# Kernel tuning notes

Measured on AMD Instinct MI355X. Metric: run time of the kernel, lower is better.

Reference implementation:

```python
import jax, jax.numpy as jnp
import numpy as np

B, S, D = 4, 2048, 1024
H, HD = 16, 64
MLP = 4 * D
EPS = 1e-6


def _rms_norm(x, scale):
    var = jnp.mean(jnp.square(x), axis=-1, keepdims=True)
    return x * jax.lax.rsqrt(var + EPS) * scale


def setup_inputs() -> dict:
    key = jax.random.key(0)
    ks = jax.random.split(key, 8)
    sd = D ** -0.5
    return {
        "x": jax.random.normal(ks[0], (B, S, D), jnp.float32),
        "pre_norm_scale": jnp.ones((D,), jnp.float32),
        "w_mlp_in": jax.random.normal(ks[1], (D, MLP), jnp.float32) * sd,   # MLPBlockInput, no bias
        "wq": jax.random.normal(ks[2], (D, H, HD), jnp.float32) * sd,
        "wk": jax.random.normal(ks[3], (D, H, HD), jnp.float32) * sd,
        "wv": jax.random.normal(ks[4], (D, H, HD), jnp.float32) * sd,
        "w_mlp_out": jax.random.normal(ks[5], (MLP, D), jnp.float32) * (MLP ** -0.5),
        "b_mlp_out": jnp.zeros((D,), jnp.float32),
        "w_attn_out": jax.random.normal(ks[6], (H, HD, D), jnp.float32) * sd,  # DenseGeneral axis=(-2,-1)
        "b_attn_out": jnp.zeros((D,), jnp.float32),
    }


def reference(x, pre_norm_scale, w_mlp_in, wq, wk, wv, w_mlp_out, b_mlp_out,
              w_attn_out, b_attn_out):
    residual = x
    xn = _rms_norm(x, pre_norm_scale)                      # pre_norm (TPNorm)

    # QKVMLPDense: fused MLP-input + QKV projections
    h = jax.nn.gelu(jnp.einsum("bsd,df->bsf", xn, w_mlp_in))   # [B,S,MLP]
    q = jnp.einsum("bsd,dhk->bshk", xn, wq)                    # [B,S,H,HD]
    k = jnp.einsum("bsd,dhk->bshk", xn, wk)
    v = jnp.einsum("bsd,dhk->bshk", xn, wv)

    # dot_product_attention (mask=None)
    scores = jnp.einsum("bqhd,bkhd->bhqk", q, k) / jnp.sqrt(jnp.asarray(HD, x.dtype))
    probs = jax.nn.softmax(scores, axis=-1)
    attn_v = jnp.einsum("bhqk,bkhd->bqhd", probs, v)           # [B,S,H,HD]

    # AttnMLPOut: mlp_out + attn_out
    mlp_out = jnp.einsum("bsf,fd->bsd", h, w_mlp_out) + b_mlp_out
    attn_out = jnp.einsum("bqhk,hkd->bqd", attn_v, w_attn_out) + b_attn_out
    block_out = mlp_out + attn_out                              # dropout is identity (train=False)
    return residual + block_out
```

## Files before the change

kernel.cpp:

```cpp
#include <hip/hip_runtime.h>
#include <cstdint>
#include <cstddef>

typedef float floatx4 __attribute__((ext_vector_type(4)));
typedef short bf16x8 __attribute__((ext_vector_type(8)));

#define MFMA(a, b, c) __builtin_amdgcn_mfma_f32_16x16x32_bf16((a), (b), (c), 0, 0, 0)

__device__ __forceinline__ unsigned short f2bf(float f) {
  union { float f; unsigned int u; } v; v.f = f;
  unsigned int u = v.u;
  unsigned int r = (u + 0x7FFFu + ((u >> 16) & 1u)) >> 16;
  return (unsigned short)r;
}

__device__ __forceinline__ void gload_lds16(const unsigned short* g, unsigned short* s) {
  __builtin_amdgcn_global_load_lds(
      (const __attribute__((address_space(1))) unsigned int*)g,
      (__attribute__((address_space(3))) unsigned int*)s, 16, 0, 0);
}

__device__ __forceinline__ float gelu_f(float v) {
  float z = 0.7978845608028654f * (v + 0.044715f * v * v * v);
  float e = __expf(2.0f * z);
  float th = 1.0f - 2.0f / (e + 1.0f);
  return 0.5f * v * (1.0f + th);
}

__global__ __launch_bounds__(256) void prep_all(
    const float* __restrict__ w_mlp_in, const float* __restrict__ wq,
    const float* __restrict__ wk, const float* __restrict__ wv,
    const float* __restrict__ w_mlp_out, const float* __restrict__ w_attn_out,
    const float* __restrict__ x, const float* __restrict__ pns,
    unsigned short* __restrict__ wcatT, unsigned short* __restrict__ wcat2T,
    unsigned short* __restrict__ xn) {
  __shared__ float tile[32][33];
  __shared__ float ws4[4];
  int id = blockIdx.x;
  if (id >= 12288) {
    int row = id - 12288;
    const float4 v = ((const float4*)(x + (size_t)row * 1024))[threadIdx.x];
    float ss = v.x * v.x + v.y * v.y + v.z * v.z + v.w * v.w;
#pragma unroll
    for (int off = 1; off < 64; off <<= 1) ss += __shfl_xor(ss, off, 64);
    if ((threadIdx.x & 63) == 0) ws4[threadIdx.x >> 6] = ss;
    __syncthreads();
    float tot = ws4[0] + ws4[1] + ws4[2] + ws4[3];
    float rs = rsqrtf(tot * (1.0f / 1024.0f) + 1e-6f);
    const float4 sc = ((const float4*)pns)[threadIdx.x];
    uint2 o;
    o.x = (unsigned)f2bf(v.x * rs * sc.x) | ((unsigned)f2bf(v.y * rs * sc.y) << 16);
    o.y = (unsigned)f2bf(v.z * rs * sc.z) | ((unsigned)f2bf(v.w * rs * sc.w) << 16);
    ((uint2*)(xn + (size_t)row * 1024))[threadIdx.x] = o;
    return;
  }
  const float* src; unsigned short* dst; int C, ldd, bx, by, q;
  if (id < 4096)       { src = w_mlp_in;   dst = wcatT;                        C = 4096; ldd = 1024; q = id;         bx = q & 127; by = q >> 7; }
  else if (id < 5120)  { src = wq;         dst = wcatT + (size_t)4096 * 1024;  C = 1024; ldd = 1024; q = id - 4096;  bx = q & 31;  by = q >> 5; }
  else if (id < 6144)  { src = wk;         dst = wcatT + (size_t)5120 * 1024;  C = 1024; ldd = 1024; q = id - 5120;  bx = q & 31;  by = q >> 5; }
  else if (id < 7168)  { src = wv;         dst = wcatT + (size_t)6144 * 1024;  C = 1024; ldd = 1024; q = id - 6144;  bx = q & 31;  by = q >> 5; }
  else if (id < 11264) { src = w_mlp_out;  dst = wcat2T;                       C = 1024; ldd = 5120; q = id - 7168;  bx = q & 31;  by = q >> 5; }
  else                 { src = w_attn_out; dst = wcat2T + 4096;                C = 1024; ldd = 5120; q = id - 11264; bx = q & 31;  by = q >> 5; }
  int tx = threadIdx.x & 31, ty = threadIdx.x >> 5;
#pragma unroll
  for (int i = 0; i < 4; i++) {
    int r = ty + i * 8;
    tile[r][tx] = src[(size_t)(by * 32 + r) * C + bx * 32 + tx];
  }
  __syncthreads();
#pragma unroll
  for (int i = 0; i < 4; i++) {
    int r = ty + i * 8;
    dst[(size_t)(bx * 32 + r) * ldd + by * 32 + tx] = f2bf(tile[tx][r]);
  }
}

template <int MODE>
__global__ __launch_bounds__(256, 2) void gemm_bt(
    const unsigned short* __restrict__ A, const unsigned short* __restrict__ BT,
    int K, void* __restrict__ outp,
    const float* __restrict__ bias1, const float* __restrict__ bias2,
    const float* __restrict__ resid,
    int msplit, int tm, int tn,
    unsigned short* __restrict__ q_out, unsigned short* __restrict__ k_out,
    unsigned short* __restrict__ v_out) {
  __shared__ unsigned short As[2][128 * 32];
  __shared__ unsigned short Bs[2][128 * 32];

  int id = blockIdx.x + gridDim.x * blockIdx.y;
  int xcd = id & 7, j = id >> 3;
  int mh = xcd % msplit, nq = xcd / msplit;
  int by = mh * tm + j / tn;
  int bx = nq * tn + j % tn;
  int m0 = by * 128, n0 = bx * 128;

  int t = threadIdx.x, lane = t & 63, wave = t >> 6;
  int l15 = lane & 15, quad = lane >> 4;
  int wm = (wave & 1) * 64, wn = (wave >> 1) * 64;

  floatx4 acc[4][4] = {};

  int lr = lane >> 2;
  int lg = (lane & 3) ^ ((lane >> 3) & 3);
  int ch0 = wave * 2, ch1 = wave * 2 + 1;
  const unsigned short* gA0 = A + (size_t)(m0 + ch0 * 16 + lr) * K + lg * 8;
  const unsigned short* gA1 = A + (size_t)(m0 + ch1 * 16 + lr) * K + lg * 8;
  const unsigned short* gB0 = BT + (size_t)(n0 + ch0 * 16 + lr) * K + lg * 8;
  const unsigned short* gB1 = BT + (size_t)(n0 + ch1 * 16 + lr) * K + lg * 8;
  unsigned short* sA0[2] = {&As[0][ch0 * 512 + lane * 8], &As[1][ch0 * 512 + lane * 8]};
  unsigned short* sA1[2] = {&As[0][ch1 * 512 + lane * 8], &As[1][ch1 * 512 + lane * 8]};
  unsigned short* sB0[2] = {&Bs[0][ch0 * 512 + lane * 8], &Bs[1][ch0 * 512 + lane * 8]};
  unsigned short* sB1[2] = {&Bs[0][ch1 * 512 + lane * 8], &Bs[1][ch1 * 512 + lane * 8]};

  int fo = (4 * l15 + (quad ^ ((l15 >> 1) & 3))) * 8;
  int ca = (wm >> 4);
  int cb = (wn >> 4);

  for (int kt = 0; kt < K; kt += 64) {
    __syncthreads();
#pragma unroll
    for (int kk = 0; kk < 2; kk++) {
      int kg = kt + kk * 32;
      gload_lds16(gA0 + kg, sA0[kk]);
      gload_lds16(gA1 + kg, sA1[kk]);
      gload_lds16(gB0 + kg, sB0[kk]);
      gload_lds16(gB1 + kg, sB1[kk]);
    }
    __syncthreads();
#pragma unroll
    for (int kk = 0; kk < 2; kk++) {
      bf16x8 a[4], b[4];
#pragma unroll
      for (int im = 0; im < 4; im++)
        a[im] = *(const bf16x8*)&As[kk][(ca + im) * 512 + fo];
#pragma unroll
      for (int in_ = 0; in_ < 4; in_++)
        b[in_] = *(const bf16x8*)&Bs[kk][(cb + in_) * 512 + fo];
#pragma unroll
      for (int im = 0; im < 4; im++)
#pragma unroll
        for (int in_ = 0; in_ < 4; in_++)
          acc[im][in_] = MFMA(a[im], b[in_], acc[im][in_]);
    }
  }

#pragma unroll
  for (int im = 0; im < 4; im++) {
#pragma unroll
    for (int in_ = 0; in_ < 4; in_++) {
      int row0 = m0 + wm + im * 16 + quad * 4;
      int col = n0 + wn + in_ * 16 + l15;
      if constexpr (MODE == 6) {
        if (n0 < 4096) {
#pragma unroll
          for (int r = 0; r < 4; r++) {
            __builtin_nontemporal_store(f2bf(gelu_f(acc[im][in_][r])),
                &((unsigned short*)outp)[(size_t)(row0 + r) * 5120 + col]);
          }
        } else {
          int seg = (n0 - 4096) >> 10;
          int cs = col - 4096 - (seg << 10);
          int h = cs >> 6, hd = cs & 63;
          int b_ = row0 >> 11, s0 = row0 & 2047;
          if (seg == 2) {
            unsigned long long o =
                (unsigned long long)((unsigned)f2bf(acc[im][in_][0]) |
                                     ((unsigned)f2bf(acc[im][in_][1]) << 16)) |
                ((unsigned long long)((unsigned)f2bf(acc[im][in_][2]) |
                                      ((unsigned)f2bf(acc[im][in_][3]) << 16)) << 32);
            __builtin_nontemporal_store(o,
                (unsigned long long*)&v_out[(((size_t)(b_ * 16 + h)) * 64 + hd) * 2048 + s0]);
          } else {
            float sc = (seg == 0) ? 0.125f : 1.0f;
            unsigned short* dst = (seg == 0) ? q_out : k_out;
#pragma unroll
            for (int r = 0; r < 4; r++) {
              __builtin_nontemporal_store(f2bf(acc[im][in_][r] * sc),
                  &dst[(((size_t)(b_ * 16 + h)) * 2048 + s0 + r) * 64 + hd]);
            }
          }
        }
      } else {
        float bsum = bias1[col] + bias2[col];
#pragma unroll
        for (int r = 0; r < 4; r++) {
          size_t idx = (size_t)(row0 + r) * 1024 + col;
          float res = __builtin_nontemporal_load(&resid[idx]);
          __builtin_nontemporal_store(acc[im][in_][r] + bsum + res, &((float*)outp)[idx]);
        }
      }
    }
  }
}

__global__ __launch_bounds__(256, 2) void flash_attn(
    const unsigned short* __restrict__ q_buf, const unsigned short* __restrict__ k_buf,
    const unsigned short* __restrict__ v_buf, unsigned short* __restrict__ cat) {
  constexpr int S = 2048, HD = 64;
  constexpr int LK = 72, LV = 72, LP = 68;
  __shared__ unsigned short Ks[64 * LK];
  __shared__ unsigned short Vs[64 * LV];
  __shared__ unsigned short Ps[4][32 * LP];

  int id = blockIdx.x + gridDim.x * blockIdx.y;
  int xcd = id & 7, j = id >> 3;
  int bh = xcd * 8 + (j >> 4);
  int qbk = j & 15;

  int t = threadIdx.x, lane = t & 63, wave = t >> 6;
  int l15 = lane & 15, quad = lane >> 4;

  const unsigned short* qp = q_buf + (size_t)bh * S * HD;
  const unsigned short* kp = k_buf + (size_t)bh * S * HD;
  const unsigned short* vp = v_buf + (size_t)bh * HD * S;

  int q0 = qbk * 128 + wave * 32;
  bf16x8 aQ[2][2];
#pragma unroll
  for (int qf = 0; qf < 2; qf++) {
    aQ[qf][0] = *(const bf16x8*)&qp[(size_t)(q0 + qf * 16 + l15) * HD + quad * 8];
    aQ[qf][1] = *(const bf16x8*)&qp[(size_t)(q0 + qf * 16 + l15) * HD + 32 + quad * 8];
  }

  floatx4 acc_o[2][4] = {};
  float lrow[2][4] = {};

  int kr = t >> 3, kc = (t & 7) * 8;

  uint4 rK0 = *(const uint4*)&kp[(size_t)kr * HD + kc];
  uint4 rK1 = *(const uint4*)&kp[(size_t)(kr + 32) * HD + kc];
  uint4 rV0 = *(const uint4*)&vp[(size_t)kr * S + kc];
  uint4 rV1 = *(const uint4*)&vp[(size_t)(kr + 32) * S + kc];

  for (int kv = 0; kv < S; kv += 64) {
    __syncthreads();
    *(uint4*)&Ks[kr * LK + kc] = rK0;
    *(uint4*)&Ks[(kr + 32) * LK + kc] = rK1;
    *(uint4*)&Vs[kr * LV + kc] = rV0;
    *(uint4*)&Vs[(kr + 32) * LV + kc] = rV1;
    __syncthreads();
    if (kv + 64 < S) {
      rK0 = *(const uint4*)&kp[(size_t)(kv + 64 + kr) * HD + kc];
      rK1 = *(const uint4*)&kp[(size_t)(kv + 64 + kr + 32) * HD + kc];
      rV0 = *(const uint4*)&vp[(size_t)kr * S + kv + 64 + kc];
      rV1 = *(const uint4*)&vp[(size_t)(kr + 32) * S + kv + 64 + kc];
    }

    floatx4 z[2][4];
#pragma unroll
    for (int cg = 0; cg < 4; cg++) {
      bf16x8 bk0 = *(const bf16x8*)&Ks[(cg * 16 + l15) * LK + quad * 8];
      bf16x8 bk1 = *(const bf16x8*)&Ks[(cg * 16 + l15) * LK + 32 + quad * 8];
#pragma unroll
      for (int qf = 0; qf < 2; qf++) {
        floatx4 acc = {};
        acc = MFMA(aQ[qf][0], bk0, acc);
        acc = MFMA(aQ[qf][1], bk1, acc);
        z[qf][cg] = acc;
      }
    }
#pragma unroll
    for (int qf = 0; qf < 2; qf++)
#pragma unroll
      for (int cg = 0; cg < 4; cg++)
#pragma unroll
        for (int r = 0; r < 4; r++) {
          float e = __expf(z[qf][cg][r]);
          lrow[qf][r] += e;
          Ps[wave][(qf * 16 + quad * 4 + r) * LP + cg * 16 + l15] = f2bf(e);
        }
    asm volatile("s_waitcnt lgkmcnt(0)" ::: "memory");
#pragma unroll
    for (int c = 0; c < 2; c++) {
      bf16x8 aP[2];
#pragma unroll
      for (int qf = 0; qf < 2; qf++) {
        const unsigned short* pp = &Ps[wave][(qf * 16 + l15) * LP + c * 32 + quad * 8];
        ((uint2*)&aP[qf])[0] = *(const uint2*)pp;
        ((uint2*)&aP[qf])[1] = *(const uint2*)(pp + 4);
      }
#pragma unroll
      for (int n = 0; n < 4; n++) {
        bf16x8 bv = *(const bf16x8*)&Vs[(n * 16 + l15) * LV + c * 32 + quad * 8];
        acc_o[0][n] = MFMA(aP[0], bv, acc_o[0][n]);
        acc_o[1][n] = MFMA(aP[1], bv, acc_o[1][n]);
      }
    }
  }

#pragma unroll
  for (int qf = 0; qf < 2; qf++)
#pragma unroll
    for (int r = 0; r < 4; r++) {
      float s = lrow[qf][r];
#pragma unroll
      for (int off = 1; off < 16; off <<= 1) s += __shfl_xor(s, off, 16);
      lrow[qf][r] = s;
    }

  int b_ = bh >> 4, h = bh & 15;
#pragma unroll
  for (int qf = 0; qf < 2; qf++)
#pragma unroll
    for (int r = 0; r < 4; r++) {
      float inv = 1.0f / lrow[qf][r];
      int srow = q0 + qf * 16 + quad * 4 + r;
      size_t base = ((size_t)(b_ * 2048 + srow)) * 5120 + 4096 + h * 64;
#pragma unroll
      for (int n = 0; n < 4; n++)
        cat[base + n * 16 + l15] = f2bf(acc_o[qf][n][r] * inv);
    }
}

extern "C" void kernel_launch(void* const* d_in, const int* in_sizes, int n_in,
                              void* d_out, int out_size, void* d_ws, size_t ws_size,
                              hipStream_t stream) {
  (void)in_sizes; (void)n_in; (void)out_size; (void)ws_size;
  const float* x          = (const float*)d_in[0];
  const float* pns        = (const float*)d_in[1];
  const float* w_mlp_in   = (const float*)d_in[2];
  const float* wq         = (const float*)d_in[3];
  const float* wk         = (const float*)d_in[4];
  const float* wv         = (const float*)d_in[5];
  const float* w_mlp_out  = (const float*)d_in[6];
  const float* b_mlp_out  = (const float*)d_in[7];
  const float* w_attn_out = (const float*)d_in[8];
  const float* b_attn_out = (const float*)d_in[9];
  float* out = (float*)d_out;

  char* ws = (char*)d_ws;
  size_t off = 0;
  auto alloc = [&](size_t bytes) {
    void* p = ws + off;
    off += (bytes + 255) & ~(size_t)255;
    return p;
  };
  const size_t M = 8192;
  unsigned short* xn     = (unsigned short*)alloc(M * 1024 * 2);
  unsigned short* wcatT  = (unsigned short*)alloc((size_t)7168 * 1024 * 2);
  unsigned short* wcat2T = (unsigned short*)alloc((size_t)1024 * 5120 * 2);
  unsigned short* cat    = (unsigned short*)alloc(M * 5120 * 2);
  unsigned short* qb     = (unsigned short*)alloc(M * 1024 * 2);
  unsigned short* kb     = (unsigned short*)alloc(M * 1024 * 2);
  unsigned short* vb     = (unsigned short*)alloc(M * 1024 * 2);

  prep_all<<<dim3(20480), 256, 0, stream>>>(
      w_mlp_in, wq, wk, wv, w_mlp_out, w_attn_out, x, pns, wcatT, wcat2T, xn);

  gemm_bt<6><<<dim3(56, 64), 256, 0, stream>>>(
      xn, wcatT, 1024, cat, nullptr, nullptr, nullptr, 2, 32, 14, qb, kb, vb);

  flash_attn<<<dim3(16, 64), 256, 0, stream>>>(qb, kb, vb, cat);

  gemm_bt<7><<<dim3(8, 64), 256, 0, stream>>>(
      cat, wcat2T, 5120, out, b_mlp_out, b_attn_out, x, 2, 32, 2, nullptr, nullptr, nullptr);
}
```

Baseline: 520.7 us.

## Split QKV GEMM out and co-schedule MLP-in GEMM with flash attention

```diff
diff --git a/kernel.cpp b/kernel.cpp
--- a/kernel.cpp
+++ b/kernel.cpp
@@ -76,6 +76,119 @@
 }
 
 template <int MODE>
+__device__ __forceinline__ void gemm_core(
+    int xcd, int j,
+    const unsigned short* __restrict__ A, const unsigned short* __restrict__ BT,
+    int K, void* __restrict__ outp,
+    const float* __restrict__ bias1, const float* __restrict__ bias2,
+    const float* __restrict__ resid,
+    int msplit, int tm, int tn,
+    unsigned short* __restrict__ q_out, unsigned short* __restrict__ k_out,
+    unsigned short* __restrict__ v_out,
+    unsigned short* As, unsigned short* Bs) {
+  int mh = xcd % msplit, nq = xcd / msplit;
+  int by = mh * tm + j / tn;
+  int bx = nq * tn + j % tn;
+  int m0 = by * 128, n0 = bx * 128;
+
+  int t = threadIdx.x, lane = t & 63, wave = t >> 6;
+  int l15 = lane & 15, quad = lane >> 4;
+  int wm = (wave & 1) * 64, wn = (wave >> 1) * 64;
+
+  floatx4 acc[4][4] = {};
+
+  int lr = lane >> 2;
+  int lg = (lane & 3) ^ ((lane >> 3) & 3);
+  int ch0 = wave * 2, ch1 = wave * 2 + 1;
+  const unsigned short* gA0 = A + (size_t)(m0 + ch0 * 16 + lr) * K + lg * 8;
+  const unsigned short* gA1 = A + (size_t)(m0 + ch1 * 16 + lr) * K + lg * 8;
+  const unsigned short* gB0 = BT + (size_t)(n0 + ch0 * 16 + lr) * K + lg * 8;
+  const unsigned short* gB1 = BT + (size_t)(n0 + ch1 * 16 + lr) * K + lg * 8;
+  unsigned short* sA0[2] = {As + ch0 * 512 + lane * 8, As + 4096 + ch0 * 512 + lane * 8};
+  unsigned short* sA1[2] = {As + ch1 * 512 + lane * 8, As + 4096 + ch1 * 512 + lane * 8};
+  unsigned short* sB0[2] = {Bs + ch0 * 512 + lane * 8, Bs + 4096 + ch0 * 512 + lane * 8};
+  unsigned short* sB1[2] = {Bs + ch1 * 512 + lane * 8, Bs + 4096 + ch1 * 512 + lane * 8};
+
+  int fo = (4 * l15 + (quad ^ ((l15 >> 1) & 3))) * 8;
+  int ca = (wm >> 4);
+  int cb = (wn >> 4);
+
+  for (int kt = 0; kt < K; kt += 64) {
+    __syncthreads();
+#pragma unroll
+    for (int kk = 0; kk < 2; kk++) {
+      int kg = kt + kk * 32;
+      gload_lds16(gA0 + kg, sA0[kk]);
+      gload_lds16(gA1 + kg, sA1[kk]);
+      gload_lds16(gB0 + kg, sB0[kk]);
+      gload_lds16(gB1 + kg, sB1[kk]);
+    }
+    __syncthreads();
+#pragma unroll
+    for (int kk = 0; kk < 2; kk++) {
+      bf16x8 a[4], b[4];
+#pragma unroll
+      for (int im = 0; im < 4; im++)
+        a[im] = *(const bf16x8*)&As[kk * 4096 + (ca + im) * 512 + fo];
+#pragma unroll
+      for (int in_ = 0; in_ < 4; in_++)
+        b[in_] = *(const bf16x8*)&Bs[kk * 4096 + (cb + in_) * 512 + fo];
+#pragma unroll
+      for (int im = 0; im < 4; im++)
+#pragma unroll
+        for (int in_ = 0; in_ < 4; in_++)
+          acc[im][in_] = MFMA(a[im], b[in_], acc[im][in_]);
+    }
+  }
+
+#pragma unroll
+  for (int im = 0; im < 4; im++) {
+#pragma unroll
+    for (int in_ = 0; in_ < 4; in_++) {
+      int row0 = m0 + wm + im * 16 + quad * 4;
+      int col = n0 + wn + in_ * 16 + l15;
+      if constexpr (MODE == 8) {
+#pragma unroll
+        for (int r = 0; r < 4; r++) {
+          __builtin_nontemporal_store(f2bf(gelu_f(acc[im][in_][r])),
+              &((unsigned short*)outp)[(size_t)(row0 + r) * 5120 + col]);
+        }
+      } else if constexpr (MODE == 9) {
+        int seg = n0 >> 10;
+        int cs = col - (seg << 10);
+        int h = cs >> 6, hd = cs & 63;
+        int b_ = row0 >> 11, s0 = row0 & 2047;
+        if (seg == 2) {
+          unsigned long long o =
+              (unsigned long long)((unsigned)f2bf(acc[im][in_][0]) |
+                                   ((unsigned)f2bf(acc[im][in_][1]) << 16)) |
+              ((unsigned long long)((unsigned)f2bf(acc[im][in_][2]) |
+                                    ((unsigned)f2bf(acc[im][in_][3]) << 16)) << 32);
+          __builtin_nontemporal_store(o,
+              (unsigned long long*)&v_out[(((size_t)(b_ * 16 + h)) * 64 + hd) * 2048 + s0]);
+        } else {
+          float sc = (seg == 0) ? 0.125f : 1.0f;
+          unsigned short* dst = (seg == 0) ? q_out : k_out;
+#pragma unroll
+          for (int r = 0; r < 4; r++) {
+            __builtin_nontemporal_store(f2bf(acc[im][in_][r] * sc),
+                &dst[(((size_t)(b_ * 16 + h)) * 2048 + s0 + r) * 64 + hd]);
+          }
+        }
+      } else {
+        float bsum = bias1[col] + bias2[col];
+#pragma unroll
+        for (int r = 0; r < 4; r++) {
+          size_t idx = (size_t)(row0 + r) * 1024 + col;
+          float res = __builtin_nontemporal_load(&resid[idx]);
+          __builtin_nontemporal_store(acc[im][in_][r] + bsum + res, &((float*)outp)[idx]);
+        }
+      }
+    }
+  }
+}
+
+template <int MODE>
 __global__ __launch_bounds__(256, 2) void gemm_bt(
     const unsigned short* __restrict__ A, const unsigned short* __restrict__ BT,
     int K, void* __restrict__ outp,
@@ -84,131 +197,30 @@
     int msplit, int tm, int tn,
     unsigned short* __restrict__ q_out, unsigned short* __restrict__ k_out,
     unsigned short* __restrict__ v_out) {
-  __shared__ unsigned short As[2][128 * 32];
-  __shared__ unsigned short Bs[2][128 * 32];
-
+  __shared__ unsigned short As[2 * 128 * 32];
+  __shared__ unsigned short Bs[2 * 128 * 32];
   int id = blockIdx.x + gridDim.x * blockIdx.y;
-  int xcd = id & 7, j = id >> 3;
-  int mh = xcd % msplit, nq = xcd / msplit;
-  int by = mh * tm + j / tn;
-  int bx = nq * tn + j % tn;
-  int m0 = by * 128, n0 = bx * 128;
+  gemm_core<MODE>(id & 7, id >> 3, A, BT, K, outp, bias1, bias2, resid,
+                  msplit, tm, tn, q_out, k_out, v_out, As, Bs);
+}
+
+__device__ __forceinline__ void flash_body(
+    int xcd, int j,
+    const unsigned short* __restrict__ q_buf, const unsigned short* __restrict__ k_buf,
+    const unsigned short* __restrict__ v_buf, unsigned short* __restrict__ cat,
+    unsigned short* smem) {
+  constexpr int S = 2048, HD = 64;
+  constexpr int LK = 72, LV = 72, LP = 68;
+  unsigned short* Ks = smem;
+  unsigned short* Vs = smem + 4608;
+  unsigned short* Psb = smem + 9216;
+
+  int bh = xcd * 8 + (j >> 4);
+  int qbk = j & 15;
 
   int t = threadIdx.x, lane = t & 63, wave = t >> 6;
   int l15 = lane & 15, quad = lane >> 4;
-  int wm = (wave & 1) * 64, wn = (wave >> 1) * 64;
-
-  floatx4 acc[4][4] = {};
-
-  int lr = lane >> 2;
-  int lg = (lane & 3) ^ ((lane >> 3) & 3);
-  int ch0 = wave * 2, ch1 = wave * 2 + 1;
-  const unsigned short* gA0 = A + (size_t)(m0 + ch0 * 16 + lr) * K + lg * 8;
-  const unsigned short* gA1 = A + (size_t)(m0 + ch1 * 16 + lr) * K + lg * 8;
-  const unsigned short* gB0 = BT + (size_t)(n0 + ch0 * 16 + lr) * K + lg * 8;
-  const unsigned short* gB1 = BT + (size_t)(n0 + ch1 * 16 + lr) * K + lg * 8;
-  unsigned short* sA0[2] = {&As[0][ch0 * 512 + lane * 8], &As[1][ch0 * 512 + lane * 8]};
-  unsigned short* sA1[2] = {&As[0][ch1 * 512 + lane * 8], &As[1][ch1 * 512 + lane * 8]};
-  unsigned short* sB0[2] = {&Bs[0][ch0 * 512 + lane * 8], &Bs[1][ch0 * 512 + lane * 8]};
-  unsigned short* sB1[2] = {&Bs[0][ch1 * 512 + lane * 8], &Bs[1][ch1 * 512 + lane * 8]};
-
-  int fo = (4 * l15 + (quad ^ ((l15 >> 1) & 3))) * 8;
-  int ca = (wm >> 4);
-  int cb = (wn >> 4);
-
-  for (int kt = 0; kt < K; kt += 64) {
-    __syncthreads();
-#pragma unroll
-    for (int kk = 0; kk < 2; kk++) {
-      int kg = kt + kk * 32;
-      gload_lds16(gA0 + kg, sA0[kk]);
-      gload_lds16(gA1 + kg, sA1[kk]);
-      gload_lds16(gB0 + kg, sB0[kk]);
-      gload_lds16(gB1 + kg, sB1[kk]);
-    }
-    __syncthreads();
-#pragma unroll
-    for (int kk = 0; kk < 2; kk++) {
-      bf16x8 a[4], b[4];
-#pragma unroll
-      for (int im = 0; im < 4; im++)
-        a[im] = *(const bf16x8*)&As[kk][(ca + im) * 512 + fo];
-#pragma unroll
-      for (int in_ = 0; in_ < 4; in_++)
-        b[in_] = *(const bf16x8*)&Bs[kk][(cb + in_) * 512 + fo];
-#pragma unroll
-      for (int im = 0; im < 4; im++)
-#pragma unroll
-        for (int in_ = 0; in_ < 4; in_++)
-          acc[im][in_] = MFMA(a[im], b[in_], acc[im][in_]);
-    }
-  }
-
-#pragma unroll
-  for (int im = 0; im < 4; im++) {
-#pragma unroll
-    for (int in_ = 0; in_ < 4; in_++) {
-      int row0 = m0 + wm + im * 16 + quad * 4;
-      int col = n0 + wn + in_ * 16 + l15;
-      if constexpr (MODE == 6) {
-        if (n0 < 4096) {
-#pragma unroll
-          for (int r = 0; r < 4; r++) {
-            __builtin_nontemporal_store(f2bf(gelu_f(acc[im][in_][r])),
-                &((unsigned short*)outp)[(size_t)(row0 + r) * 5120 + col]);
-          }
-        } else {
-          int seg = (n0 - 4096) >> 10;
-          int cs = col - 4096 - (seg << 10);
-          int h = cs >> 6, hd = cs & 63;
-          int b_ = row0 >> 11, s0 = row0 & 2047;
-          if (seg == 2) {
-            unsigned long long o =
-                (unsigned long long)((unsigned)f2bf(acc[im][in_][0]) |
-                                     ((unsigned)f2bf(acc[im][in_][1]) << 16)) |
-                ((unsigned long long)((unsigned)f2bf(acc[im][in_][2]) |
-                                      ((unsigned)f2bf(acc[im][in_][3]) << 16)) << 32);
-            __builtin_nontemporal_store(o,
-                (unsigned long long*)&v_out[(((size_t)(b_ * 16 + h)) * 64 + hd) * 2048 + s0]);
-          } else {
-            float sc = (seg == 0) ? 0.125f : 1.0f;
-            unsigned short* dst = (seg == 0) ? q_out : k_out;
-#pragma unroll
-            for (int r = 0; r < 4; r++) {
-              __builtin_nontemporal_store(f2bf(acc[im][in_][r] * sc),
-                  &dst[(((size_t)(b_ * 16 + h)) * 2048 + s0 + r) * 64 + hd]);
-            }
-          }
-        }
-      } else {
-        float bsum = bias1[col] + bias2[col];
-#pragma unroll
-        for (int r = 0; r < 4; r++) {
-          size_t idx = (size_t)(row0 + r) * 1024 + col;
-          float res = __builtin_nontemporal_load(&resid[idx]);
-          __builtin_nontemporal_store(acc[im][in_][r] + bsum + res, &((float*)outp)[idx]);
-        }
-      }
-    }
-  }
-}
-
-__global__ __launch_bounds__(256, 2) void flash_attn(
-    const unsigned short* __restrict__ q_buf, const unsigned short* __restrict__ k_buf,
-    const unsigned short* __restrict__ v_buf, unsigned short* __restrict__ cat) {
-  constexpr int S = 2048, HD = 64;
-  constexpr int LK = 72, LV = 72, LP = 68;
-  __shared__ unsigned short Ks[64 * LK];
-  __shared__ unsigned short Vs[64 * LV];
-  __shared__ unsigned short Ps[4][32 * LP];
-
-  int id = blockIdx.x + gridDim.x * blockIdx.y;
-  int xcd = id & 7, j = id >> 3;
-  int bh = xcd * 8 + (j >> 4);
-  int qbk = j & 15;
-
-  int t = threadIdx.x, lane = t & 63, wave = t >> 6;
-  int l15 = lane & 15, quad = lane >> 4;
+  unsigned short* Ps = Psb + wave * (32 * LP);
 
   const unsigned short* qp = q_buf + (size_t)bh * S * HD;
   const unsigned short* kp = k_buf + (size_t)bh * S * HD;
@@ -267,7 +279,7 @@
         for (int r = 0; r < 4; r++) {
           float e = __expf(z[qf][cg][r]);
           lrow[qf][r] += e;
-          Ps[wave][(qf * 16 + quad * 4 + r) * LP + cg * 16 + l15] = f2bf(e);
+          Ps[(qf * 16 + quad * 4 + r) * LP + cg * 16 + l15] = f2bf(e);
         }
     asm volatile("s_waitcnt lgkmcnt(0)" ::: "memory");
 #pragma unroll
@@ -275,7 +287,7 @@
       bf16x8 aP[2];
 #pragma unroll
       for (int qf = 0; qf < 2; qf++) {
-        const unsigned short* pp = &Ps[wave][(qf * 16 + l15) * LP + c * 32 + quad * 8];
+        const unsigned short* pp = &Ps[(qf * 16 + l15) * LP + c * 32 + quad * 8];
         ((uint2*)&aP[qf])[0] = *(const uint2*)pp;
         ((uint2*)&aP[qf])[1] = *(const uint2*)(pp + 4);
       }
@@ -310,6 +322,23 @@
       for (int n = 0; n < 4; n++)
         cat[base + n * 16 + l15] = f2bf(acc_o[qf][n][r] * inv);
     }
+}
+
+__global__ __launch_bounds__(256, 2) void fused_mlp_attn(
+    const unsigned short* __restrict__ xn, const unsigned short* __restrict__ wcatT,
+    unsigned short* __restrict__ cat,
+    const unsigned short* __restrict__ qb, const unsigned short* __restrict__ kb,
+    const unsigned short* __restrict__ vb) {
+  __shared__ __align__(16) unsigned short smem[17920];
+  int phys = blockIdx.x;
+  int xcd = phys & 7, r = phys >> 3;
+  if (r % 3 == 2) {
+    flash_body(xcd, r / 3, qb, kb, vb, cat, smem);
+  } else {
+    int g = (r / 3) * 2 + (r % 3);
+    gemm_core<8>(xcd, g, xn, wcatT, 1024, cat, nullptr, nullptr, nullptr,
+                 2, 32, 8, nullptr, nullptr, nullptr, smem, smem + 8192);
+  }
 }
 
 extern "C" void kernel_launch(void* const* d_in, const int* in_sizes, int n_in,
@@ -347,10 +376,11 @@
   prep_all<<<dim3(20480), 256, 0, stream>>>(
       w_mlp_in, wq, wk, wv, w_mlp_out, w_attn_out, x, pns, wcatT, wcat2T, xn);
 
-  gemm_bt<6><<<dim3(56, 64), 256, 0, stream>>>(
-      xn, wcatT, 1024, cat, nullptr, nullptr, nullptr, 2, 32, 14, qb, kb, vb);
-
-  flash_attn<<<dim3(16, 64), 256, 0, stream>>>(qb, kb, vb, cat);
+  gemm_bt<9><<<dim3(1536), 256, 0, stream>>>(
+      xn, wcatT + (size_t)4096 * 1024, 1024, nullptr, nullptr, nullptr, nullptr,
+      2, 32, 6, qb, kb, vb);
+
+  fused_mlp_attn<<<dim3(3072), 256, 0, stream>>>(xn, wcatT, cat, qb, kb, vb);
 
   gemm_bt<7><<<dim3(8, 64), 256, 0, stream>>>(
       cat, wcat2T, 5120, out, b_mlp_out, b_attn_out, x, 2, 32, 2, nullptr, nullptr, nullptr);
```

New measurement: 538.6 us. +3.4%, slower.
